# Optimization experiments

Measured on AMD Instinct MI355X. Metric: run time of the kernel, lower is better.

## Reference

```python
import jax, jax.numpy as jnp
import numpy as np

THRESHOLD = 0.5
SLACK = 3
EPS = 1e-12
B, H, W = 16, 512, 512


def _shift(p, dy, dx, b, h, w):
    # p is zero-padded by 1 on spatial dims; returns neighbor at offset (dy, dx)
    return p[:, 1 + dy:1 + dy + h, 1 + dx:1 + dx + w]


def _thin_sub(img, step):
    # One Zhang-Suen sub-iteration on bool image [B,H,W] (zero boundary, as skimage)
    b, h, w = img.shape
    p = jnp.pad(img.astype(jnp.int32), ((0, 0), (1, 1), (1, 1)))
    # P2..P9 clockwise starting at North
    P2 = _shift(p, -1, 0, b, h, w); P3 = _shift(p, -1, 1, b, h, w)
    P4 = _shift(p, 0, 1, b, h, w);  P5 = _shift(p, 1, 1, b, h, w)
    P6 = _shift(p, 1, 0, b, h, w);  P7 = _shift(p, 1, -1, b, h, w)
    P8 = _shift(p, 0, -1, b, h, w); P9 = _shift(p, -1, -1, b, h, w)
    seq = [P2, P3, P4, P5, P6, P7, P8, P9, P2]
    Bn = P2 + P3 + P4 + P5 + P6 + P7 + P8 + P9          # neighbor count
    A = sum((1 - seq[k]) * seq[k + 1] for k in range(8))  # 0->1 transitions
    cond = (Bn >= 2) & (Bn <= 6) & (A == 1)
    if step == 0:
        cond = cond & (P2 * P4 * P6 == 0) & (P4 * P6 * P8 == 0)
    else:
        cond = cond & (P2 * P4 * P8 == 0) & (P2 * P6 * P8 == 0)
    return img & ~cond


def _skeletonize(img):
    # Iterate Zhang-Suen thinning to convergence (skimage.morphology.skeletonize 2D = Zhang's method)
    def body(state):
        cur, _ = state
        nxt = _thin_sub(_thin_sub(cur, 0), 1)
        return (nxt, jnp.any(nxt != cur))

    out, _ = jax.lax.while_loop(lambda s: s[1], body, (img, jnp.array(True)))
    return out


def _edt_sq(mask):
    # Exact squared Euclidean distance to nearest True pixel, separable 2-pass.
    b, h, w = mask.shape
    BIG = h + w  # larger than any attainable 1D distance
    g = jnp.where(mask, 0, BIG).astype(jnp.int32)  # [B,H,W]

    # pass 1: 1D nearest-True distance along rows (axis=1) via fwd/bwd scans
    def fscan(carry, row):
        d = jnp.minimum(row, carry + 1)
        return d, d

    g_rows = jnp.moveaxis(g, 1, 0)  # [H,B,W]
    init = jnp.full((b, w), BIG, jnp.int32)
    _, fwd = jax.lax.scan(fscan, init, g_rows)
    _, bwd = jax.lax.scan(fscan, init, g_rows[::-1])
    f = jnp.minimum(jnp.minimum(fwd, bwd[::-1]), BIG)  # [H,B,W]
    f2 = jnp.moveaxis(f * f, 0, 1)  # [B,H,W] squared vertical distance

    # pass 2: d2[b,i,j] = min_{j'} f2[b,i,j'] + (j-j')^2 (lower envelope, memory-friendly lax.map)
    js = jnp.arange(w, dtype=jnp.int32)

    def one_col(j):
        off = (js - j) ** 2  # [W]
        return jnp.min(f2 + off[None, None, :], axis=-1)  # [B,H]

    d2 = jax.lax.map(one_col, js)  # [W,B,H]
    return jnp.transpose(d2, (1, 2, 0))  # [B,H,W]


def setup_inputs() -> dict:
    key = jax.random.key(0)
    k1, k2 = jax.random.split(key)
    y_pred = jax.random.uniform(k1, (B, H, W), dtype=jnp.float32)
    y_true = jax.random.uniform(k2, (B, H, W), dtype=jnp.float32)
    return {"y_pred": y_pred, "y_true": y_true}


def reference(y_pred, y_true):
    p = y_pred > THRESHOLD  # greater_is_road=True binarization
    g = y_true > THRESHOLD
    p = _skeletonize(p)
    g = _skeletonize(g)
    d2_gt = _edt_sq(g)   # EDT of ~g == distance to nearest g pixel
    d2_pr = _edt_sq(p)
    s2 = SLACK * SLACK   # dist <= slack  <=>  dist^2 <= slack^2 (integer sq EDT)
    tp_area = d2_gt <= s2
    fp_area = ~tp_area
    fn_area = d2_pr > s2
    ax = (1, 2)
    TP = jnp.sum(tp_area & p, ax).astype(jnp.float32)
    FP = jnp.sum(fp_area & p, ax).astype(jnp.float32)
    FN = jnp.sum(fn_area & g, ax).astype(jnp.float32)
    correctness = TP / (TP + FP + EPS)
    completeness = TP / (TP + FN + EPS)
    quality = TP / (TP + FP + FN + EPS)
    # mean over batch -> [3]: [correctness, completeness, quality]
    return jnp.mean(jnp.stack([correctness, completeness, quality], axis=1), axis=0)
```

## Files before the change

### kernel.cpp

```cpp
#include <hip/hip_runtime.h>
#include <stdint.h>

#define HH 512
#define WW 512
#define WPR 8
#define NWORDS (HH * WPR)
#define NTHREADS 1024
#define WPT (NWORDS / NTHREADS)
#define NB 16

typedef unsigned long long u64;

__device__ __forceinline__ u64 ldw(const u64* M, int r, int c) {
    return (r < 0 || r >= HH || c < 0 || c >= WPR) ? 0ULL : M[r * WPR + c];
}

__device__ __forceinline__ u64 zs_word(const u64* M, int r, int c, int step) {
    u64 nm = ldw(M, r - 1, c - 1), nc = ldw(M, r - 1, c), np = ldw(M, r - 1, c + 1);
    u64 cm = ldw(M, r,     c - 1), cc = ldw(M, r,     c), cp = ldw(M, r,     c + 1);
    u64 sm = ldw(M, r + 1, c - 1), sc = ldw(M, r + 1, c), sp = ldw(M, r + 1, c + 1);

    u64 P2 = nc;
    u64 P3 = (nc >> 1) | (np << 63);
    u64 P4 = (cc >> 1) | (cp << 63);
    u64 P5 = (sc >> 1) | (sp << 63);
    u64 P6 = sc;
    u64 P7 = (sc << 1) | (sm >> 63);
    u64 P8 = (cc << 1) | (cm >> 63);
    u64 P9 = (nc << 1) | (nm >> 63);

    u64 ab = P2 ^ P3;
    u64 s1 = ab ^ P4, c1 = (P2 & P3) | (ab & P4);
    u64 de = P5 ^ P6;
    u64 s2 = de ^ P7, c2 = (P5 & P6) | (de & P7);
    u64 s3 = P8 ^ P9, c3 = P8 & P9;
    u64 gh = s1 ^ s2;
    u64 b0 = gh ^ s3, c4 = (s1 & s2) | (gh & s3);
    u64 ij = c1 ^ c2;
    u64 s4 = ij ^ c3, c5 = (c1 & c2) | (ij & c3);
    u64 b1 = s4 ^ c4, c6 = s4 & c4;
    u64 b2 = c5 ^ c6, b3 = c5 & c6;

    u64 Bge2 = b1 | b2 | b3;
    u64 Ble6 = ~(b3 | (b2 & b1 & b0));

    u64 a1, a2, t;
    t = ~P2 & P3; a1 = t; a2 = 0ULL;
    t = ~P3 & P4; a2 |= a1 & t; a1 |= t;
    t = ~P4 & P5; a2 |= a1 & t; a1 |= t;
    t = ~P5 & P6; a2 |= a1 & t; a1 |= t;
    t = ~P6 & P7; a2 |= a1 & t; a1 |= t;
    t = ~P7 & P8; a2 |= a1 & t; a1 |= t;
    t = ~P8 & P9; a2 |= a1 & t; a1 |= t;
    t = ~P9 & P2; a2 |= a1 & t; a1 |= t;
    u64 Aeq1 = a1 & ~a2;

    u64 sccond;
    if (step == 0) sccond = ~(P2 & P4 & P6) & ~(P4 & P6 & P8);
    else           sccond = ~(P2 & P4 & P8) & ~(P2 & P6 & P8);

    return cc & ~(Bge2 & Ble6 & Aeq1 & sccond);
}

__global__ __launch_bounds__(NTHREADS)
void skel_kernel(const float* __restrict__ y_pred,
                 const float* __restrict__ y_true,
                 u64* __restrict__ skel ,
                 int* __restrict__ cnt ) {
    __shared__ u64 M[NWORDS];
    __shared__ unsigned int Cp[HH + 2];
    __shared__ int s_any[2];

    int bx = blockIdx.x;
    int tid = threadIdx.x;
    int lane = tid & 63;

    if (bx == 0 && tid < 4 * NB) cnt[tid] = 0;

    const float* src = (bx < NB) ? y_pred + (size_t)bx * HH * WW
                                 : y_true + (size_t)(bx - NB) * HH * WW;

    {
        unsigned short* M16 = (unsigned short*)M;
        const float4* s4 = (const float4*)src;
        #pragma unroll
        for (int i = 0; i < 16; ++i) {
            int t = i * NTHREADS + tid;
            float4 a = s4[t * 4 + 0];
            float4 b = s4[t * 4 + 1];
            float4 c = s4[t * 4 + 2];
            float4 d = s4[t * 4 + 3];
            unsigned bits =
                ((unsigned)(a.x > 0.5f) << 0)  | ((unsigned)(a.y > 0.5f) << 1)  |
                ((unsigned)(a.z > 0.5f) << 2)  | ((unsigned)(a.w > 0.5f) << 3)  |
                ((unsigned)(b.x > 0.5f) << 4)  | ((unsigned)(b.y > 0.5f) << 5)  |
                ((unsigned)(b.z > 0.5f) << 6)  | ((unsigned)(b.w > 0.5f) << 7)  |
                ((unsigned)(c.x > 0.5f) << 8)  | ((unsigned)(c.y > 0.5f) << 9)  |
                ((unsigned)(c.z > 0.5f) << 10) | ((unsigned)(c.w > 0.5f) << 11) |
                ((unsigned)(d.x > 0.5f) << 12) | ((unsigned)(d.y > 0.5f) << 13) |
                ((unsigned)(d.z > 0.5f) << 14) | ((unsigned)(d.w > 0.5f) << 15);
            M16[t] = (unsigned short)bits;
        }
    }

    for (int i = tid; i < HH + 2; i += NTHREADS)
        Cp[i] = (i >= 1 && i <= HH) ? 0x1FEu : 0u;
    if (tid < 2) s_any[tid] = 0;

    unsigned dl[WPT];
    #pragma unroll
    for (int k = 0; k < WPT; ++k) dl[k] = 0x1FEu;

    int p = 0;
    for (;;) {
        for (int step = 0; step < 2; ++step) {
            __syncthreads();
            u64 nv[WPT];
            u64 bal[WPT];
            bool anyc = false;
            #pragma unroll
            for (int k = 0; k < WPT; ++k) {
                int wi = k * NTHREADS + tid;
                int r = wi >> 3, c = wi & 7;
                unsigned need = ((Cp[r] | Cp[r + 1] | Cp[r + 2]) >> c) & 7u;
                bool chg = false;
                u64 x = 0;
                if (need) {
                    u64 cur = M[wi];
                    x = zs_word(M, r, c, step);
                    chg = (x != cur);
                }
                nv[k] = x;
                bal[k] = __ballot(chg);
                anyc |= (bal[k] != 0);
            }
            __syncthreads();
            #pragma unroll
            for (int k = 0; k < WPT; ++k) {
                int wi = k * NTHREADS + tid;
                if ((bal[k] >> lane) & 1) M[wi] = nv[k];
                if ((lane & 7) == 0) {
                    unsigned byte = ((unsigned)(bal[k] >> lane) & 0xFFu) << 1;
                    int idx = (wi >> 3) + 1;
                    Cp[idx] = byte | dl[k];
                    dl[k] = byte;
                }
            }
            if (anyc) s_any[p] = 1;
        }
        __syncthreads();
        int done = (s_any[p] == 0);
        if (tid == 0) s_any[p ^ 1] = 0;
        p ^= 1;
        if (done) break;
    }

    u64* dst = skel + (size_t)bx * NWORDS;
    #pragma unroll
    for (int k = 0; k < WPT; ++k) {
        int wi = k * NTHREADS + tid;
        dst[wi] = M[wi];
    }
}

#define STRIPS 8
#define SROWS (HH / STRIPS)
#define SR2 (SROWS + 6)

__device__ __forceinline__ u64 ldws(const u64* M, int r, int c) {
    return (c < 0 || c >= WPR) ? 0ULL : M[r * WPR + c];
}

__device__ __forceinline__ u64 dil3s(const u64* M, int r, int c) {
    u64 cm = ldws(M, r, c - 1), cc = ldws(M, r, c), cp = ldws(M, r, c + 1);
    u64 h = cc
          | (cc >> 1) | (cp << 63)
          | (cc >> 2) | (cp << 62)
          | (cc >> 3) | (cp << 61)
          | (cc << 1) | (cm >> 63)
          | (cc << 2) | (cm >> 62)
          | (cc << 3) | (cm >> 61);
    u64 um = ldws(M, r - 1, c - 1) | ldws(M, r + 1, c - 1) | ldws(M, r - 2, c - 1) | ldws(M, r + 2, c - 1);
    u64 uc = ldws(M, r - 1, c    ) | ldws(M, r + 1, c    ) | ldws(M, r - 2, c    ) | ldws(M, r + 2, c    );
    u64 up = ldws(M, r - 1, c + 1) | ldws(M, r + 1, c + 1) | ldws(M, r - 2, c + 1) | ldws(M, r + 2, c + 1);
    h |= uc
       | (uc >> 1) | (up << 63)
       | (uc >> 2) | (up << 62)
       | (uc << 1) | (um >> 63)
       | (uc << 2) | (um >> 62);
    h |= ldws(M, r - 3, c) | ldws(M, r + 3, c);
    return h;
}

__global__ __launch_bounds__(256)
void count_kernel(const u64* __restrict__ skel, int* __restrict__ cnt) {
    __shared__ u64 P[SR2 * WPR];
    __shared__ u64 G[SR2 * WPR];
    __shared__ int acc[4];

    int b = blockIdx.x / STRIPS;
    int s = blockIdx.x % STRIPS;
    int tid = threadIdx.x;
    int r0 = s * SROWS - 3;

    const u64* sp = skel + (size_t)b * NWORDS;
    const u64* sg = skel + (size_t)(NB + b) * NWORDS;
    for (int i = tid; i < SR2 * WPR; i += 256) {
        int gr = r0 + (i >> 3);
        bool in = (gr >= 0 && gr < HH);
        int gi = gr * WPR + (i & 7);
        P[i] = in ? sp[gi] : 0ULL;
        G[i] = in ? sg[gi] : 0ULL;
    }
    if (tid < 4) acc[tid] = 0;
    __syncthreads();

    int cp = 0, cg = 0, tp = 0, fnh = 0;
    #pragma unroll
    for (int k = 0; k < 2; ++k) {
        int w = k * 256 + tid;
        int r = (w >> 3) + 3, c = w & 7;
        u64 pw = P[r * WPR + c], gw = G[r * WPR + c];
        cp  += __popcll(pw);
        cg  += __popcll(gw);
        tp  += __popcll(pw & dil3s(G, r, c));
        fnh += __popcll(gw & dil3s(P, r, c));
    }
    #pragma unroll
    for (int o = 32; o > 0; o >>= 1) {
        cp  += __shfl_down(cp, o);
        cg  += __shfl_down(cg, o);
        tp  += __shfl_down(tp, o);
        fnh += __shfl_down(fnh, o);
    }
    if ((tid & 63) == 0) {
        atomicAdd(&acc[0], cp);
        atomicAdd(&acc[1], cg);
        atomicAdd(&acc[2], tp);
        atomicAdd(&acc[3], fnh);
    }
    __syncthreads();
    if (tid < 4) atomicAdd(&cnt[b * 4 + tid], acc[tid]);
}

__global__ void ccq_reduce(const int* __restrict__ cnt, float* __restrict__ out) {
    int k = threadIdx.x;
    if (k < 3) {
        float s = 0.0f;
        for (int b = 0; b < NB; ++b) {
            float TP = (float)cnt[b * 4 + 2];
            float FP = (float)(cnt[b * 4 + 0] - cnt[b * 4 + 2]);
            float FN = (float)(cnt[b * 4 + 1] - cnt[b * 4 + 3]);
            float v = (k == 0) ? TP / (TP + FP + 1e-12f)
                    : (k == 1) ? TP / (TP + FN + 1e-12f)
                               : TP / (TP + FP + FN + 1e-12f);
            s += v;
        }
        out[k] = s * (1.0f / NB);
    }
}

extern "C" void kernel_launch(void* const* d_in, const int* in_sizes, int n_in,
                              void* d_out, int out_size, void* d_ws, size_t ws_size,
                              hipStream_t stream) {
    (void)in_sizes; (void)n_in; (void)out_size; (void)ws_size;
    const float* y_pred = (const float*)d_in[0];
    const float* y_true = (const float*)d_in[1];
    float* out = (float*)d_out;

    u64* skel = (u64*)d_ws;
    int* cnt = (int*)((char*)d_ws + (size_t)2 * NB * NWORDS * sizeof(u64));

    hipLaunchKernelGGL(skel_kernel, dim3(2 * NB), dim3(NTHREADS), 0, stream,
                       y_pred, y_true, skel, cnt);
    hipLaunchKernelGGL(count_kernel, dim3(NB * STRIPS), dim3(256), 0, stream,
                       skel, cnt);
    hipLaunchKernelGGL(ccq_reduce, dim3(1), dim3(64), 0, stream, cnt, out);
}
```

Before: 131.3 us.

## Split float binarization into a grid-wide pack kernel before skeletonization

Moves thresholding and bit-packing of the float inputs out of the 32-block skeleton kernel into a separate 512-block pack kernel that uses wave ballots, so the 32 MB input read is spread across the whole GPU instead of only 32 CUs. The skeleton kernel then loads the packed bitmask from the workspace and writes its result back in place. The count kernel is split into twice as many strips with one word per thread. This adds a kernel launch and a small extra round trip of the packed mask through global memory.

Result: no change. 132.9 us (+1.2%).

```diff
diff --git a/kernel.cpp b/kernel.cpp
--- a/kernel.cpp
+++ b/kernel.cpp
@@ -8,6 +8,7 @@
 #define NTHREADS 1024
 #define WPT (NWORDS / NTHREADS)
 #define NB 16
+#define NMASK (2 * NB)
 
 typedef unsigned long long u64;
 
@@ -62,11 +63,29 @@
     return cc & ~(Bge2 & Ble6 & Aeq1 & sccond);
 }
 
+__global__ __launch_bounds__(256)
+void pack_kernel(const float* __restrict__ y_pred,
+                 const float* __restrict__ y_true,
+                 u64* __restrict__ bits ,
+                 int* __restrict__ cnt ) {
+    if (blockIdx.x == 0 && threadIdx.x < 4 * NB) cnt[threadIdx.x] = 0;
+    int gw = (blockIdx.x * 256 + threadIdx.x) >> 6;
+    int lane = threadIdx.x & 63;
+    int wbase = gw * 64;
+    #pragma unroll 4
+    for (int it = 0; it < 64; ++it) {
+        int wi = wbase + it;
+        int img = wi >> 12;
+        const float* src = (img < NB) ? y_pred + (size_t)img * (HH * WW)
+                                      : y_true + (size_t)(img - NB) * (HH * WW);
+        float v = src[((wi & (NWORDS - 1)) << 6) + lane];
+        u64 w = __ballot(v > 0.5f);
+        if (lane == 0) bits[wi] = w;
+    }
+}
+
 __global__ __launch_bounds__(NTHREADS)
-void skel_kernel(const float* __restrict__ y_pred,
-                 const float* __restrict__ y_true,
-                 u64* __restrict__ skel ,
-                 int* __restrict__ cnt ) {
+void skel_kernel(u64* __restrict__ bits ) {
     __shared__ u64 M[NWORDS];
     __shared__ unsigned int Cp[HH + 2];
     __shared__ int s_any[2];
@@ -74,33 +93,12 @@
     int bx = blockIdx.x;
     int tid = threadIdx.x;
     int lane = tid & 63;
-
-    if (bx == 0 && tid < 4 * NB) cnt[tid] = 0;
-
-    const float* src = (bx < NB) ? y_pred + (size_t)bx * HH * WW
-                                 : y_true + (size_t)(bx - NB) * HH * WW;
-
-    {
-        unsigned short* M16 = (unsigned short*)M;
-        const float4* s4 = (const float4*)src;
-        #pragma unroll
-        for (int i = 0; i < 16; ++i) {
-            int t = i * NTHREADS + tid;
-            float4 a = s4[t * 4 + 0];
-            float4 b = s4[t * 4 + 1];
-            float4 c = s4[t * 4 + 2];
-            float4 d = s4[t * 4 + 3];
-            unsigned bits =
-                ((unsigned)(a.x > 0.5f) << 0)  | ((unsigned)(a.y > 0.5f) << 1)  |
-                ((unsigned)(a.z > 0.5f) << 2)  | ((unsigned)(a.w > 0.5f) << 3)  |
-                ((unsigned)(b.x > 0.5f) << 4)  | ((unsigned)(b.y > 0.5f) << 5)  |
-                ((unsigned)(b.z > 0.5f) << 6)  | ((unsigned)(b.w > 0.5f) << 7)  |
-                ((unsigned)(c.x > 0.5f) << 8)  | ((unsigned)(c.y > 0.5f) << 9)  |
-                ((unsigned)(c.z > 0.5f) << 10) | ((unsigned)(c.w > 0.5f) << 11) |
-                ((unsigned)(d.x > 0.5f) << 12) | ((unsigned)(d.y > 0.5f) << 13) |
-                ((unsigned)(d.z > 0.5f) << 14) | ((unsigned)(d.w > 0.5f) << 15);
-            M16[t] = (unsigned short)bits;
-        }
+    u64* mine = bits + (size_t)bx * NWORDS;
+
+    #pragma unroll
+    for (int k = 0; k < WPT; ++k) {
+        int wi = k * NTHREADS + tid;
+        M[wi] = mine[wi];
     }
 
     for (int i = tid; i < HH + 2; i += NTHREADS)
@@ -155,15 +153,14 @@
         if (done) break;
     }
 
-    u64* dst = skel + (size_t)bx * NWORDS;
     #pragma unroll
     for (int k = 0; k < WPT; ++k) {
         int wi = k * NTHREADS + tid;
-        dst[wi] = M[wi];
-    }
-}
-
-#define STRIPS 8
+        mine[wi] = M[wi];
+    }
+}
+
+#define STRIPS 16
 #define SROWS (HH / STRIPS)
 #define SR2 (SROWS + 6)
 
@@ -193,7 +190,7 @@
 }
 
 __global__ __launch_bounds__(256)
-void count_kernel(const u64* __restrict__ skel, int* __restrict__ cnt) {
+void count_kernel(const u64* __restrict__ bits, int* __restrict__ cnt) {
     __shared__ u64 P[SR2 * WPR];
     __shared__ u64 G[SR2 * WPR];
     __shared__ int acc[4];
@@ -203,8 +200,8 @@
     int tid = threadIdx.x;
     int r0 = s * SROWS - 3;
 
-    const u64* sp = skel + (size_t)b * NWORDS;
-    const u64* sg = skel + (size_t)(NB + b) * NWORDS;
+    const u64* sp = bits + (size_t)b * NWORDS;
+    const u64* sg = bits + (size_t)(NB + b) * NWORDS;
     for (int i = tid; i < SR2 * WPR; i += 256) {
         int gr = r0 + (i >> 3);
         bool in = (gr >= 0 && gr < HH);
@@ -215,17 +212,13 @@
     if (tid < 4) acc[tid] = 0;
     __syncthreads();
 
-    int cp = 0, cg = 0, tp = 0, fnh = 0;
-    #pragma unroll
-    for (int k = 0; k < 2; ++k) {
-        int w = k * 256 + tid;
-        int r = (w >> 3) + 3, c = w & 7;
-        u64 pw = P[r * WPR + c], gw = G[r * WPR + c];
-        cp  += __popcll(pw);
-        cg  += __popcll(gw);
-        tp  += __popcll(pw & dil3s(G, r, c));
-        fnh += __popcll(gw & dil3s(P, r, c));
-    }
+    int r = (tid >> 3) + 3, c = tid & 7;
+    u64 pw = P[r * WPR + c], gw = G[r * WPR + c];
+    int cp  = __popcll(pw);
+    int cg  = __popcll(gw);
+    int tp  = __popcll(pw & dil3s(G, r, c));
+    int fnh = __popcll(gw & dil3s(P, r, c));
+
     #pragma unroll
     for (int o = 32; o > 0; o >>= 1) {
         cp  += __shfl_down(cp, o);
@@ -268,12 +261,13 @@
     const float* y_true = (const float*)d_in[1];
     float* out = (float*)d_out;
 
-    u64* skel = (u64*)d_ws;
-    int* cnt = (int*)((char*)d_ws + (size_t)2 * NB * NWORDS * sizeof(u64));
-
-    hipLaunchKernelGGL(skel_kernel, dim3(2 * NB), dim3(NTHREADS), 0, stream,
-                       y_pred, y_true, skel, cnt);
+    u64* bits = (u64*)d_ws;
+    int* cnt = (int*)((char*)d_ws + (size_t)NMASK * NWORDS * sizeof(u64));
+
+    hipLaunchKernelGGL(pack_kernel, dim3(512), dim3(256), 0, stream,
+                       y_pred, y_true, bits, cnt);
+    hipLaunchKernelGGL(skel_kernel, dim3(NMASK), dim3(NTHREADS), 0, stream, bits);
     hipLaunchKernelGGL(count_kernel, dim3(NB * STRIPS), dim3(256), 0, stream,
-                       skel, cnt);
+                       bits, cnt);
     hipLaunchKernelGGL(ccq_reduce, dim3(1), dim3(64), 0, stream, cnt, out);
 }
```
